# Performance work log

Measured on AMD Instinct MI355X. Metric: run time of the kernel, lower is better.

Reference implementation:

```python
import jax, jax.numpy as jnp
import numpy as np

INPUT_SIZE = 256
OUTPUT_SIZE = 128
N = 8192
SLOPE = 0.01
NEG_BIG = -9e15


def setup_inputs() -> dict:
    key = jax.random.key(0)
    k_h, k_adj, k_W, k_a = jax.random.split(key, 4)
    h = jax.random.normal(k_h, (N, INPUT_SIZE), dtype=jnp.float32)
    adj = jax.random.randint(k_adj, (N, N), 0, 2, dtype=jnp.int32)
    # xavier_uniform with gain=1.414
    gain = 1.414
    lim_W = gain * np.sqrt(6.0 / (INPUT_SIZE + OUTPUT_SIZE))
    W = jax.random.uniform(k_W, (INPUT_SIZE, OUTPUT_SIZE), dtype=jnp.float32, minval=-lim_W, maxval=lim_W)
    lim_a = gain * np.sqrt(6.0 / (2 * OUTPUT_SIZE + 1))
    a = jax.random.uniform(k_a, (2 * OUTPUT_SIZE, 1), dtype=jnp.float32, minval=-lim_a, maxval=lim_a)
    return {"h": h, "adj": adj, "W": W, "a": a}


def reference(h, adj, W, a):
    # Wh: [N, F]
    Wh = h @ W
    Fo = Wh.shape[1]
    # Original builds [N, N, 2F] concat then matmul with a; equivalent to
    # e[i, j] = leaky_relu(Wh[i] . a[:F] + Wh[j] . a[F:]) via broadcasting.
    src = Wh @ a[:Fo, 0]   # [N]
    dst = Wh @ a[Fo:, 0]   # [N]
    e = jax.nn.leaky_relu(src[:, None] + dst[None, :], negative_slope=SLOPE)  # [N, N]
    att = jnp.where(adj > 0, e, NEG_BIG)
    att = jax.nn.softmax(att, axis=1)
    return att @ Wh
```

## Files before the change

kernel.cpp:

```cpp
#include <hip/hip_runtime.h>
#include <hip/hip_bf16.h>

typedef unsigned short u16;
typedef unsigned int u32;
typedef __attribute__((ext_vector_type(8))) short short8;
typedef __attribute__((ext_vector_type(4))) float f32x4;

#define NN 8192
#define KIN 256
#define FOUT 128
#define SPLITS 8
#define KPER (NN / SPLITS)
#define BK 64
#define ITERS (KPER / BK)

__device__ __forceinline__ u16 f2bf(float f) {
    u32 u = __float_as_uint(f);
    u32 r = ((u >> 16) & 1u) + 0x7fffu;
    return (u16)((u + r) >> 16);
}
__device__ __forceinline__ u32 fkey(float f) {
    u32 b = __float_as_uint(f);
    return (b & 0x80000000u) ? ~b : (b | 0x80000000u);
}
__device__ __forceinline__ float funkey(u32 k) {
    u32 b = (k & 0x80000000u) ? (k & 0x7fffffffu) : ~k;
    return __uint_as_float(b);
}

__global__ __launch_bounds__(256) void k1_wh(
    const float* __restrict__ h, const float* __restrict__ W, const float* __restrict__ a,
    u16* __restrict__ whbt,
    float* __restrict__ src, float* __restrict__ dst, u32* __restrict__ gmaxk)
{
    __shared__ float hT[64][36];
    __shared__ u16   lt[128][40];
    __shared__ float sd[32][2];
    const int t  = threadIdx.x;
    const int m0 = blockIdx.x * 32;
    const int rq = t >> 5, cq = t & 31;

    float acc[4][4];
#pragma unroll
    for (int i = 0; i < 4; i++)
#pragma unroll
        for (int j = 0; j < 4; j++) acc[i][j] = 0.f;
    if (t < 64) sd[t >> 1][t & 1] = 0.f;

    for (int kt = 0; kt < KIN; kt += 64) {
        __syncthreads();
#pragma unroll
        for (int s2 = 0; s2 < 2; s2++) {
            int f = s2 * 256 + t;
            int r = f >> 4, kc = (f & 15) * 4;
            float4 hv = *(const float4*)(h + (size_t)(m0 + r) * KIN + kt + kc);
            hT[kc + 0][r] = hv.x; hT[kc + 1][r] = hv.y;
            hT[kc + 2][r] = hv.z; hT[kc + 3][r] = hv.w;
        }
        __syncthreads();
        for (int k = 0; k < 64; k++) {
            float4 wv = *(const float4*)(W + (size_t)(kt + k) * FOUT + cq * 4);
            float h0 = hT[k][rq * 4 + 0], h1 = hT[k][rq * 4 + 1];
            float h2 = hT[k][rq * 4 + 2], h3 = hT[k][rq * 4 + 3];
            acc[0][0] += h0 * wv.x; acc[0][1] += h0 * wv.y; acc[0][2] += h0 * wv.z; acc[0][3] += h0 * wv.w;
            acc[1][0] += h1 * wv.x; acc[1][1] += h1 * wv.y; acc[1][2] += h1 * wv.z; acc[1][3] += h1 * wv.w;
            acc[2][0] += h2 * wv.x; acc[2][1] += h2 * wv.y; acc[2][2] += h2 * wv.z; acc[2][3] += h2 * wv.w;
            acc[3][0] += h3 * wv.x; acc[3][1] += h3 * wv.y; acc[3][2] += h3 * wv.z; acc[3][3] += h3 * wv.w;
        }
    }
#pragma unroll
    for (int i = 0; i < 4; i++) {
        float sp = 0.f, dp = 0.f;
#pragma unroll
        for (int j = 0; j < 4; j++) {
            sp += acc[i][j] * a[cq * 4 + j];
            dp += acc[i][j] * a[FOUT + cq * 4 + j];
            lt[cq * 4 + j][rq * 4 + i] = f2bf(acc[i][j]);
        }
        atomicAdd(&sd[rq * 4 + i][0], sp);
        atomicAdd(&sd[rq * 4 + i][1], dp);
    }
    __syncthreads();
    if (t < 32) { src[m0 + t] = sd[t][0]; dst[m0 + t] = sd[t][1]; }
    if (t < 64) {
        float v = (t < 32) ? sd[t][1] : -3.0e38f;
#pragma unroll
        for (int off = 32; off >= 1; off >>= 1) v = fmaxf(v, __shfl_down(v, off));
        if (t == 0) atomicMax(gmaxk, fkey(v));
    }
#pragma unroll
    for (int s2 = 0; s2 < 2; s2++) {
        int f = s2 * 256 + t;
        int n = f >> 2;
        int q = (f & 3) * 8;
        uint4 v = *(const uint4*)&lt[n][q];
        *(uint4*)(whbt + (size_t)n * NN + m0 + q) = v;
    }
}

__global__ __launch_bounds__(256) void k2_attn(
    const int* __restrict__ adj, const float* __restrict__ src, const float* __restrict__ dst,
    const u16* __restrict__ whbt, const u32* __restrict__ gmaxk,
    float* __restrict__ accp, float* __restrict__ lp)
{
    __shared__ u16 P[128][72];
    __shared__ float2 sC[128];
    __shared__ float lred[128][16];
    const int t = threadIdx.x;
    const int i0 = blockIdx.x * 128;
    const int split = blockIdx.y;
    const int kb0 = split * KPER;
    const int lane = t & 63, wave = t >> 6;
    const int mw = (wave >> 1) * 64, nw = (wave & 1) * 64;
    const int l15 = lane & 15, quad = lane >> 4;
    const int g = t >> 4, c4 = (t & 15) * 4;

    if (t < 128) {
        float s = src[i0 + t];
        float gm = funkey(*gmaxk);
        float x = s + gm;
        sC[t] = make_float2(s, fmaxf(x, 0.01f * x));
    }
    float psum[8];
#pragma unroll
    for (int s2 = 0; s2 < 8; s2++) psum[s2] = 0.f;
    f32x4 acc[4][4];
#pragma unroll
    for (int mt = 0; mt < 4; mt++)
#pragma unroll
        for (int nt = 0; nt < 4; nt++) acc[mt][nt] = {0.f, 0.f, 0.f, 0.f};

    int4 av[8]; float4 dv;
    dv = *(const float4*)(dst + kb0 + c4);
#pragma unroll
    for (int s2 = 0; s2 < 8; s2++)
        av[s2] = *(const int4*)(adj + (size_t)(i0 + 16 * s2 + g) * NN + kb0 + c4);

    for (int it = 0; it < ITERS; ++it) {
        const int kb = kb0 + it * BK;
        __syncthreads();
        float4 d4 = dv;
#pragma unroll
        for (int s2 = 0; s2 < 8; s2++) {
            int r = 16 * s2 + g;
            float2 sc = sC[r];
            int4 a4 = av[s2];
            float x0 = sc.x + d4.x; x0 = fmaxf(x0, 0.01f * x0);
            float x1 = sc.x + d4.y; x1 = fmaxf(x1, 0.01f * x1);
            float x2 = sc.x + d4.z; x2 = fmaxf(x2, 0.01f * x2);
            float x3 = sc.x + d4.w; x3 = fmaxf(x3, 0.01f * x3);
            float p0 = (a4.x > 0) ? __expf(x0 - sc.y) : 0.f;
            float p1 = (a4.y > 0) ? __expf(x1 - sc.y) : 0.f;
            float p2 = (a4.z > 0) ? __expf(x2 - sc.y) : 0.f;
            float p3 = (a4.w > 0) ? __expf(x3 - sc.y) : 0.f;
            psum[s2] += (p0 + p1) + (p2 + p3);
            u32 lo = (u32)f2bf(p0) | ((u32)f2bf(p1) << 16);
            u32 hi = (u32)f2bf(p2) | ((u32)f2bf(p3) << 16);
            *(uint2*)&P[r][c4] = make_uint2(lo, hi);
        }
        __syncthreads();
        if (it + 1 < ITERS) {
            int kbn = kb + BK;
            dv = *(const float4*)(dst + kbn + c4);
#pragma unroll
            for (int s2 = 0; s2 < 8; s2++)
                av[s2] = *(const int4*)(adj + (size_t)(i0 + 16 * s2 + g) * NN + kbn + c4);
        }
#pragma unroll
        for (int ks = 0; ks < 2; ks++) {
            int kk = ks * 32 + quad * 8;
            short8 af[4], bfr[4];
#pragma unroll
            for (int mt = 0; mt < 4; mt++)
                af[mt] = *(const short8*)&P[mw + mt * 16 + l15][kk];
#pragma unroll
            for (int nt = 0; nt < 4; nt++) {
                int n = nw + nt * 16 + l15;
                bfr[nt] = *(const short8*)(whbt + (size_t)n * NN + kb + kk);
            }
#pragma unroll
            for (int mt = 0; mt < 4; mt++)
#pragma unroll
                for (int nt = 0; nt < 4; nt++)
                    acc[mt][nt] = __builtin_amdgcn_mfma_f32_16x16x32_bf16(
                        af[mt], bfr[nt], acc[mt][nt], 0, 0, 0);
        }
    }
    __syncthreads();
#pragma unroll
    for (int s2 = 0; s2 < 8; s2++) lred[16 * s2 + g][t & 15] = psum[s2];
    __syncthreads();
    if (t < 128) {
        float s = 0.f;
#pragma unroll
        for (int j = 0; j < 16; j++) s += lred[t][j];
        lp[split * NN + i0 + t] = s;
    }
    float* ab = accp + (size_t)split * (NN * FOUT);
#pragma unroll
    for (int mt = 0; mt < 4; mt++)
#pragma unroll
        for (int nt = 0; nt < 4; nt++) {
            int row = i0 + mw + mt * 16 + quad * 4;
            int col = nw + nt * 16 + l15;
#pragma unroll
            for (int reg = 0; reg < 4; reg++)
                ab[(size_t)(row + reg) * FOUT + col] = acc[mt][nt][reg];
        }
}

__global__ __launch_bounds__(256) void k3_comb(
    const float* __restrict__ accp, const float* __restrict__ lp, float* __restrict__ out)
{
    int idx = blockIdx.x * 256 + threadIdx.x;
    int i = idx >> 5;
    float4 s = make_float4(0.f, 0.f, 0.f, 0.f);
    float l = 0.f;
#pragma unroll
    for (int sp = 0; sp < SPLITS; sp++) {
        float4 v = *(const float4*)(accp + (size_t)sp * (NN * FOUT) + (size_t)idx * 4);
        s.x += v.x; s.y += v.y; s.z += v.z; s.w += v.w;
        l += lp[sp * NN + i];
    }
    float inv = 1.0f / l;
    *(float4*)(out + (size_t)idx * 4) = make_float4(s.x * inv, s.y * inv, s.z * inv, s.w * inv);
}

extern "C" void kernel_launch(void* const* d_in, const int* in_sizes, int n_in,
                              void* d_out, int out_size, void* d_ws, size_t ws_size,
                              hipStream_t stream) {
    const float* h   = (const float*)d_in[0];
    const int*   adj = (const int*)d_in[1];
    const float* W   = (const float*)d_in[2];
    const float* a   = (const float*)d_in[3];
    float* out = (float*)d_out;

    char* ws = (char*)d_ws;
    u16*   whbt  = (u16*)ws;
    float* src   = (float*)(ws + (2u << 20));
    float* dst   = src + NN;
    u32*   gmaxk = (u32*)(dst + NN);
    float* accp  = (float*)(ws + (3u << 20));
    float* lp    = (float*)(ws + (35u << 20));

    hipMemsetAsync(gmaxk, 0, sizeof(u32), stream);
    k1_wh<<<dim3(NN / 32), dim3(256), 0, stream>>>(h, W, a, whbt, src, dst, gmaxk);
    k2_attn<<<dim3(NN / 128, SPLITS), dim3(256), 0, stream>>>(adj, src, dst, whbt, gmaxk, accp, lp);
    k3_comb<<<dim3((NN * FOUT / 4) / 256), dim3(256), 0, stream>>>(accp, lp, out);
}
```

Measured before the change: 461.7 us.

## Stage Wh^T tile through LDS with register prefetch and use exp2

```diff
diff --git a/kernel.cpp b/kernel.cpp
--- a/kernel.cpp
+++ b/kernel.cpp
@@ -13,6 +13,9 @@
 #define KPER (NN / SPLITS)
 #define BK 64
 #define ITERS (KPER / BK)
+#define L2E 1.4426950408889634f
+
+__device__ __forceinline__ float exp2fast(float x) { return __builtin_amdgcn_exp2f(x); }
 
 __device__ __forceinline__ u16 f2bf(float f) {
     u32 u = __float_as_uint(f);
@@ -98,12 +101,13 @@
     }
 }
 
-__global__ __launch_bounds__(256) void k2_attn(
+__global__ __launch_bounds__(256, 2) void k2_attn(
     const int* __restrict__ adj, const float* __restrict__ src, const float* __restrict__ dst,
     const u16* __restrict__ whbt, const u32* __restrict__ gmaxk,
     float* __restrict__ accp, float* __restrict__ lp)
 {
     __shared__ u16 P[128][72];
+    __shared__ u16 Bs[128][72];
     __shared__ float2 sC[128];
     __shared__ float lred[128][16];
     const int t = threadIdx.x;
@@ -116,8 +120,8 @@
     const int g = t >> 4, c4 = (t & 15) * 4;
 
     if (t < 128) {
-        float s = src[i0 + t];
-        float gm = funkey(*gmaxk);
+        float s = src[i0 + t] * L2E;
+        float gm = funkey(*gmaxk) * L2E;
         float x = s + gm;
         sC[t] = make_float2(s, fmaxf(x, 0.01f * x));
     }
@@ -130,11 +134,20 @@
 #pragma unroll
         for (int nt = 0; nt < 4; nt++) acc[mt][nt] = {0.f, 0.f, 0.f, 0.f};
 
-    int4 av[8]; float4 dv;
-    dv = *(const float4*)(dst + kb0 + c4);
+    int4 av[8]; float4 dv; uint4 bv[4];
+    {
+        float4 d = *(const float4*)(dst + kb0 + c4);
+        dv = make_float4(d.x * L2E, d.y * L2E, d.z * L2E, d.w * L2E);
+    }
 #pragma unroll
     for (int s2 = 0; s2 < 8; s2++)
         av[s2] = *(const int4*)(adj + (size_t)(i0 + 16 * s2 + g) * NN + kb0 + c4);
+#pragma unroll
+    for (int p = 0; p < 4; p++) {
+        int f = p * 256 + t;
+        int n = f >> 3, seg = (f & 7) * 8;
+        bv[p] = *(const uint4*)(whbt + (size_t)n * NN + kb0 + seg);
+    }
 
     for (int it = 0; it < ITERS; ++it) {
         const int kb = kb0 + it * BK;
@@ -149,22 +162,35 @@
             float x1 = sc.x + d4.y; x1 = fmaxf(x1, 0.01f * x1);
             float x2 = sc.x + d4.z; x2 = fmaxf(x2, 0.01f * x2);
             float x3 = sc.x + d4.w; x3 = fmaxf(x3, 0.01f * x3);
-            float p0 = (a4.x > 0) ? __expf(x0 - sc.y) : 0.f;
-            float p1 = (a4.y > 0) ? __expf(x1 - sc.y) : 0.f;
-            float p2 = (a4.z > 0) ? __expf(x2 - sc.y) : 0.f;
-            float p3 = (a4.w > 0) ? __expf(x3 - sc.y) : 0.f;
+            float p0 = (a4.x > 0) ? exp2fast(x0 - sc.y) : 0.f;
+            float p1 = (a4.y > 0) ? exp2fast(x1 - sc.y) : 0.f;
+            float p2 = (a4.z > 0) ? exp2fast(x2 - sc.y) : 0.f;
+            float p3 = (a4.w > 0) ? exp2fast(x3 - sc.y) : 0.f;
             psum[s2] += (p0 + p1) + (p2 + p3);
             u32 lo = (u32)f2bf(p0) | ((u32)f2bf(p1) << 16);
             u32 hi = (u32)f2bf(p2) | ((u32)f2bf(p3) << 16);
             *(uint2*)&P[r][c4] = make_uint2(lo, hi);
         }
+#pragma unroll
+        for (int p = 0; p < 4; p++) {
+            int f = p * 256 + t;
+            int n = f >> 3, seg = (f & 7) * 8;
+            *(uint4*)&Bs[n][seg] = bv[p];
+        }
         __syncthreads();
         if (it + 1 < ITERS) {
             int kbn = kb + BK;
-            dv = *(const float4*)(dst + kbn + c4);
+            float4 d = *(const float4*)(dst + kbn + c4);
+            dv = make_float4(d.x * L2E, d.y * L2E, d.z * L2E, d.w * L2E);
 #pragma unroll
             for (int s2 = 0; s2 < 8; s2++)
                 av[s2] = *(const int4*)(adj + (size_t)(i0 + 16 * s2 + g) * NN + kbn + c4);
+#pragma unroll
+            for (int p = 0; p < 4; p++) {
+                int f = p * 256 + t;
+                int n = f >> 3, seg = (f & 7) * 8;
+                bv[p] = *(const uint4*)(whbt + (size_t)n * NN + kbn + seg);
+            }
         }
 #pragma unroll
         for (int ks = 0; ks < 2; ks++) {
@@ -174,10 +200,8 @@
             for (int mt = 0; mt < 4; mt++)
                 af[mt] = *(const short8*)&P[mw + mt * 16 + l15][kk];
 #pragma unroll
-            for (int nt = 0; nt < 4; nt++) {
-                int n = nw + nt * 16 + l15;
-                bfr[nt] = *(const short8*)(whbt + (size_t)n * NN + kb + kk);
-            }
+            for (int nt = 0; nt < 4; nt++)
+                bfr[nt] = *(const short8*)&Bs[nw + nt * 16 + l15][kk];
 #pragma unroll
             for (int mt = 0; mt < 4; mt++)
 #pragma unroll
@@ -243,7 +267,7 @@
     float* accp  = (float*)(ws + (3u << 20));
     float* lp    = (float*)(ws + (35u << 20));
 
-    hipMemsetAsync(gmaxk, 0, sizeof(u32), stream);
+    (void)hipMemsetAsync(gmaxk, 0, sizeof(u32), stream);
     k1_wh<<<dim3(NN / 32), dim3(256), 0, stream>>>(h, W, a, whbt, src, dst, gmaxk);
     k2_attn<<<dim3(NN / 128, SPLITS), dim3(256), 0, stream>>>(adj, src, dst, whbt, gmaxk, accp, lp);
     k3_comb<<<dim3((NN * FOUT / 4) / 256), dim3(256), 0, stream>>>(accp, lp, out);
```

Measured after the change: 482.4 us. +4.5%, slower.
